# Optimization experiments

Hardware: AMD Instinct MI355X
Metric: run time of the kernel (lower is better)

Reference implementation:

```python
import jax, jax.numpy as jnp
import numpy as np

B, S, D_IN, D_H, D_OUT = 4, 2048, 512, 512, 512


def setup_inputs() -> dict:
    key = jax.random.key(0)
    ks = jax.random.split(key, 11)
    s_in = 1.0 / np.sqrt(D_IN)
    s_cat = 1.0 / np.sqrt(3 * D_H)
    return {
        "x1": jax.random.normal(ks[0], (B, S, D_IN), jnp.float32),
        "x2": jax.random.normal(ks[1], (B, S, D_IN), jnp.float32),
        "x3": jax.random.normal(ks[2], (B, S, D_IN), jnp.float32),
        "Wq": jax.random.normal(ks[3], (D_IN, D_H), jnp.float32) * s_in,
        "bq": jnp.zeros((D_H,), jnp.float32),
        "Wk": jax.random.normal(ks[4], (D_IN, D_H), jnp.float32) * s_in,
        "bk": jnp.zeros((D_H,), jnp.float32),
        "Wv": jax.random.normal(ks[5], (D_IN, D_H), jnp.float32) * s_in,
        "bv": jnp.zeros((D_H,), jnp.float32),
        "Wo": jax.random.normal(ks[6], (3 * D_H, D_OUT), jnp.float32) * s_cat,
        "bo": jnp.zeros((D_OUT,), jnp.float32),
    }


def _attn(Q, K, V):
    # Q: [B,S,H], K/V: [B,S,H] -> [B,S,H]
    scale = 1.0 / jnp.sqrt(jnp.asarray(K.shape[-1], Q.dtype))
    scores = jnp.einsum('bqh,bkh->bqk', Q, K) * scale
    w = jax.nn.softmax(scores, axis=-1)
    return jnp.einsum('bqk,bkh->bqh', w, V)


def reference(x1, x2, x3, Wq, bq, Wk, bk, Wv, bv, Wo, bo):
    Q1, Q2, Q3 = x1 @ Wq + bq, x2 @ Wq + bq, x3 @ Wq + bq
    K1, K2, K3 = x1 @ Wk + bk, x2 @ Wk + bk, x3 @ Wk + bk
    V1, V2, V3 = x1 @ Wv + bv, x2 @ Wv + bv, x3 @ Wv + bv
    fused_x1 = _attn(Q1, K2, V2) + _attn(Q1, K3, V3)
    fused_x2 = _attn(Q2, K1, V1) + _attn(Q2, K3, V3)
    fused_x3 = _attn(Q3, K1, V1) + _attn(Q3, K2, V2)
    fused = jnp.concatenate([fused_x1, fused_x2, fused_x3], axis=-1)
    return fused @ Wo + bo
```

## Files before the change

kernel.cpp:

```cpp
#include <hip/hip_runtime.h>
#include <hip/hip_bf16.h>

typedef __attribute__((ext_vector_type(4))) float  f32x4;
typedef __attribute__((ext_vector_type(8))) short  short8;

#define GAS(p) ((const __attribute__((address_space(1))) void*)(p))
#define LAS(p) ((__attribute__((address_space(3))) void*)(p))

__device__ inline short bf16_of(float f) {
    union { float f; unsigned u; } v; v.f = f;
    unsigned r = v.u + 0x7FFFu + ((v.u >> 16) & 1u);
    return (short)(r >> 16);
}

#define MFMA __builtin_amdgcn_mfma_f32_16x16x32_bf16

__device__ __forceinline__ void stage64(const short* A, long lda,
                                        const short* B, long ldb,
                                        short* As, short* Bs) {
    const int tid = threadIdx.x;
    const int w = tid >> 6, l = tid & 63;
    const int r = l >> 3;
    const int scol = ((l & 7) ^ r) * 8;
#pragma unroll
    for (int q = 0; q < 4; ++q) {
        const int rowb = q * 32 + w * 8;
        __builtin_amdgcn_global_load_lds(GAS(A + (long)(rowb + r) * lda + scol),
                                         LAS(As + rowb * 64), 16, 0, 0);
        __builtin_amdgcn_global_load_lds(GAS(B + (long)(rowb + r) * ldb + scol),
                                         LAS(Bs + rowb * 64), 16, 0, 0);
    }
}

__device__ __forceinline__ void gemm_core64(const short* A, long lda,
                                            const short* B, long ldb, int nk,
                                            short* sA, short* sB,
                                            f32x4 acc[4][4]) {
    const int tid = threadIdx.x;
    const int lane = tid & 63, wid = tid >> 6;
    const int wr = wid >> 1, wc = wid & 1;
    const int fr = lane & 15, fk = lane >> 4;
    const int swz = (fr & 7) << 4;
    const int abase = (wr * 64 + fr) * 128 + fk * 16;
    const int bbase = (wc * 64 + fr) * 128 + fk * 16;

    stage64(A, lda, B, ldb, sA, sB);
    __syncthreads();
    for (int ks = 0; ks < nk; ++ks) {
        const int cur = ks & 1;
        if (ks + 1 < nk)
            stage64(A + (ks + 1) * 64, lda, B + (ks + 1) * 64, ldb,
                    sA + (cur ^ 1) * 8192, sB + (cur ^ 1) * 8192);
        const char* pa = (const char*)(sA + cur * 8192);
        const char* pb = (const char*)(sB + cur * 8192);
        short8 af[2][4], bfr[2][4];
#pragma unroll
        for (int kk = 0; kk < 2; ++kk) {
#pragma unroll
            for (int mi = 0; mi < 4; ++mi)
                af[kk][mi] = *(const short8*)(pa + (((abase + kk * 64) ^ swz) + mi * 2048));
#pragma unroll
            for (int ni = 0; ni < 4; ++ni)
                bfr[kk][ni] = *(const short8*)(pb + (((bbase + kk * 64) ^ swz) + ni * 2048));
        }
#pragma unroll
        for (int kk = 0; kk < 2; ++kk)
#pragma unroll
            for (int mi = 0; mi < 4; ++mi)
#pragma unroll
                for (int ni = 0; ni < 4; ++ni)
                    acc[mi][ni] = MFMA(af[kk][mi], bfr[kk][ni], acc[mi][ni], 0, 0, 0);
        __syncthreads();
    }
}

__device__ __forceinline__ void bounce_store(short* Pb, const short vals[4][4][4],
                                             short* C, long ldc) {
    const int tid = threadIdx.x, lane = tid & 63, wid = tid >> 6;
    const int wr = wid >> 1, wc = wid & 1, fr = lane & 15, fk = lane >> 4;
#pragma unroll
    for (int mi = 0; mi < 4; ++mi)
#pragma unroll
        for (int ni = 0; ni < 4; ++ni)
#pragma unroll
            for (int r = 0; r < 4; ++r) {
                const int row = wr * 64 + mi * 16 + fk * 4 + r;
                const int col = wc * 64 + ni * 16 + fr;
                Pb[row * 128 + (col ^ ((row & 7) << 3))] = vals[mi][ni][r];
            }
    __syncthreads();
#pragma unroll
    for (int i = 0; i < 8; ++i) {
        const int row = i * 16 + (tid >> 4);
        const int ch = tid & 15;
        short8 v = *(const short8*)&Pb[row * 128 + ((ch * 8) ^ ((row & 7) << 3))];
        *(short8*)&C[(long)row * ldc + ch * 8] = v;
    }
}

__global__ __launch_bounds__(256, 2)
void proj_qk_k(const short* __restrict__ xb, const short* __restrict__ WqkT,
               short* __restrict__ Qb, short* __restrict__ Kb,
               const float* __restrict__ bq, const float* __restrict__ bk) {
    __shared__ short sA[2 * 8192], sB[2 * 8192];
    const short* Ab = xb + (long)blockIdx.x * 128 * 512;
    const short* Bb = WqkT + (long)blockIdx.y * 128 * 512;
    f32x4 acc[4][4] = {};
    gemm_core64(Ab, 512, Bb, 512, 8, sA, sB, acc);

    const int lane = threadIdx.x & 63, wid = threadIdx.x >> 6;
    const int wc = wid & 1, fr = lane & 15;
    const int qc0 = blockIdx.y * 128;
    const float* bias = qc0 < 512 ? bq + qc0 : bk + (qc0 - 512);
    short vals[4][4][4];
#pragma unroll
    for (int mi = 0; mi < 4; ++mi)
#pragma unroll
        for (int ni = 0; ni < 4; ++ni) {
            const float bv_ = bias[wc * 64 + ni * 16 + fr];
#pragma unroll
            for (int r = 0; r < 4; ++r)
                vals[mi][ni][r] = bf16_of(acc[mi][ni][r] + bv_);
        }
    short* dst = (qc0 < 512 ? Qb + qc0 : Kb + (qc0 - 512)) + (long)blockIdx.x * 128 * 512;
    bounce_store(sA, vals, dst, 512);
}

__global__ __launch_bounds__(256, 2)
void proj_vt_k(const short* __restrict__ WvT, const short* __restrict__ xb,
               short* __restrict__ VT, const float* __restrict__ bv) {
    __shared__ short sA[2 * 8192], sB[2 * 8192];
    const short* Ab = WvT + (long)blockIdx.x * 128 * 512;
    const short* Bb = xb + (long)blockIdx.y * 128 * 512;
    f32x4 acc[4][4] = {};
    gemm_core64(Ab, 512, Bb, 512, 8, sA, sB, acc);

    const int lane = threadIdx.x & 63, wid = threadIdx.x >> 6;
    const int wr = wid >> 1, fk = lane >> 4;
    short vals[4][4][4];
#pragma unroll
    for (int mi = 0; mi < 4; ++mi)
#pragma unroll
        for (int ni = 0; ni < 4; ++ni)
#pragma unroll
            for (int r = 0; r < 4; ++r) {
                const int rowg = blockIdx.x * 128 + wr * 64 + mi * 16 + fk * 4 + r;
                vals[mi][ni][r] = bf16_of(acc[mi][ni][r] + bv[rowg]);
            }
    bounce_store(sA, vals, VT + (long)blockIdx.x * 128 * 24576 + blockIdx.y * 128, 24576);
}

struct Off6 { long a[6], b[6]; };

__global__ __launch_bounds__(256, 4)
void qk_exp(const short* __restrict__ Qb, const short* __restrict__ Kb,
            short* __restrict__ Sc, float* __restrict__ lpart,
            Off6 o, int z0, int zmask, int zshift, float kscale) {
    __shared__ short lds[16384];
    short* As = lds;
    short* Bs = lds + 8192;
    const int bid = blockIdx.x;
    const int z = bid & zmask;
    const int t = bid >> zshift;
    const int bx = t & 15, by = t >> 4;
    const int slice = z0 + z;
    const int gp = slice >> 2, b = slice & 3;
    const short* A = Qb + o.a[gp] + ((long)b * 2048 + (long)bx * 128) * 512;
    const short* B = Kb + o.b[gp] + ((long)b * 2048 + (long)by * 128) * 512;

    const int tid = threadIdx.x, lane = tid & 63, wid = tid >> 6;
    const int wr = wid >> 1, wc = wid & 1, fr = lane & 15, fk = lane >> 4;
    const int sr = tid >> 2;
    const int scc = (((tid & 3) ^ (sr & 3)) * 8);
    const int arow = wr * 64 + fr, brow = wc * 64 + fr;

    auto stage = [&](const short* Ap, const short* Bp, int cur) {
        short* ad = As + cur * 4096;
        short* bd = Bs + cur * 4096;
        __builtin_amdgcn_global_load_lds(GAS(Ap + (long)sr * 512 + scc),
                                         LAS(ad + sr * 32 + (tid & 3) * 8), 16, 0, 0);
        __builtin_amdgcn_global_load_lds(GAS(Ap + (long)(sr + 64) * 512 + scc),
                                         LAS(ad + (sr + 64) * 32 + (tid & 3) * 8), 16, 0, 0);
        __builtin_amdgcn_global_load_lds(GAS(Bp + (long)sr * 512 + scc),
                                         LAS(bd + sr * 32 + (tid & 3) * 8), 16, 0, 0);
        __builtin_amdgcn_global_load_lds(GAS(Bp + (long)(sr + 64) * 512 + scc),
                                         LAS(bd + (sr + 64) * 32 + (tid & 3) * 8), 16, 0, 0);
    };

    f32x4 acc[4][4] = {};
    stage(A, B, 0);
    __syncthreads();
    for (int ks = 0; ks < 16; ++ks) {
        const int cur = ks & 1;
        if (ks + 1 < 16) stage(A + (ks + 1) * 32, B + (ks + 1) * 32, cur ^ 1);
        const short* pa = As + cur * 4096;
        const short* pb = Bs + cur * 4096;
        short8 af[4], bf[4];
#pragma unroll
        for (int mi = 0; mi < 4; ++mi) {
            const int row = arow + mi * 16;
            af[mi] = *(const short8*)&pa[row * 32 + ((fk ^ (row & 3)) * 8)];
        }
#pragma unroll
        for (int ni = 0; ni < 4; ++ni) {
            const int row = brow + ni * 16;
            bf[ni] = *(const short8*)&pb[row * 32 + ((fk ^ (row & 3)) * 8)];
        }
#pragma unroll
        for (int mi = 0; mi < 4; ++mi)
#pragma unroll
            for (int ni = 0; ni < 4; ++ni)
                acc[mi][ni] = MFMA(af[mi], bf[ni], acc[mi][ni], 0, 0, 0);
        __syncthreads();
    }

#pragma unroll
    for (int mi = 0; mi < 4; ++mi)
#pragma unroll
        for (int ni = 0; ni < 4; ++ni)
#pragma unroll
            for (int r = 0; r < 4; ++r)
                acc[mi][ni][r] = exp2f(acc[mi][ni][r] * kscale);

#pragma unroll
    for (int mi = 0; mi < 4; ++mi)
#pragma unroll
        for (int r = 0; r < 4; ++r) {
            float s = acc[mi][0][r] + acc[mi][1][r] + acc[mi][2][r] + acc[mi][3][r];
            s += __shfl_xor(s, 1); s += __shfl_xor(s, 2);
            s += __shfl_xor(s, 4); s += __shfl_xor(s, 8);
            if (fr == 0)
                lpart[((long)z * 32 + by * 2 + wc) * 2048 +
                      (long)bx * 128 + wr * 64 + mi * 16 + fk * 4 + r] = s;
        }

    short vals[4][4][4];
#pragma unroll
    for (int mi = 0; mi < 4; ++mi)
#pragma unroll
        for (int ni = 0; ni < 4; ++ni)
#pragma unroll
            for (int r = 0; r < 4; ++r)
                vals[mi][ni][r] = bf16_of(acc[mi][ni][r]);

    short* Cb = Sc + (long)z * 2048 * 2048 +
                (long)bx * 128 * 2048 + (long)by * 128;
    bounce_store(lds, vals, Cb, 2048);
}

struct POff { long v[6], c[6]; };

__global__ __launch_bounds__(256, 2)
void pv_div(const short* __restrict__ Sc, const short* __restrict__ VT,
            const float* __restrict__ lpart, short* __restrict__ F,
            POff o, int z0, int zmask, int zshift) {
    __shared__ short sA[2 * 8192], sB[2 * 8192];
    const int bid = blockIdx.x;
    const int z = bid & zmask;
    const int t = bid >> zshift;
    const int bx = t & 15, by = t >> 4;
    const int slice = z0 + z;
    const int gp = slice >> 2, b = slice & 3;
    const short* Ab = Sc + (long)z * 2048 * 2048 + (long)bx * 128 * 2048;
    const short* Bb = VT + o.v[gp] + (long)b * 2048 + (long)by * 128 * 24576;
    f32x4 acc[4][4] = {};
    gemm_core64(Ab, 2048, Bb, 24576, 32, sA, sB, acc);

    const int tid = threadIdx.x, lane = tid & 63, wid = tid >> 6;
    const int wr = wid >> 1, wc = wid & 1, fr = lane & 15, fk = lane >> 4;

    float* linv_s = (float*)sB;
    if (tid < 128) {
        const float* lp = lpart + ((long)z * 32) * 2048 + (long)bx * 128 + tid;
        float s = 0.f;
#pragma unroll
        for (int j = 0; j < 32; ++j) s += lp[(long)j * 2048];
        linv_s[tid] = 1.0f / s;
    }
    __syncthreads();

    short vals[4][4][4];
#pragma unroll
    for (int mi = 0; mi < 4; ++mi) {
        float linv[4];
#pragma unroll
        for (int r = 0; r < 4; ++r) linv[r] = linv_s[wr * 64 + mi * 16 + fk * 4 + r];
#pragma unroll
        for (int ni = 0; ni < 4; ++ni)
#pragma unroll
            for (int r = 0; r < 4; ++r)
                vals[mi][ni][r] = bf16_of(acc[mi][ni][r] * linv[r]);
    }
    __syncthreads();

    short* Cb = F + ((long)b * 2048 + (long)bx * 128) * 3072 +
                o.c[gp] + (long)by * 128;
    bounce_store(sA, vals, Cb, 3072);
}

__device__ __forceinline__ void stage_f(const short* A, const short* B,
                                        short* As, short* Bs) {
    const int tid = threadIdx.x, w = tid >> 6, l = tid & 63;
    const int r = l >> 3, scol = ((l & 7) ^ r) * 8;
#pragma unroll
    for (int q = 0; q < 4; ++q) {
        const int rowb = q * 32 + w * 8;
        __builtin_amdgcn_global_load_lds(GAS(A + (long)(rowb + r) * 3072 + scol),
                                         LAS(As + rowb * 64), 16, 0, 0);
    }
#pragma unroll
    for (int q = 0; q < 2; ++q) {
        const int rowb = q * 32 + w * 8;
        __builtin_amdgcn_global_load_lds(GAS(B + (long)(rowb + r) * 3072 + scol),
                                         LAS(Bs + rowb * 64), 16, 0, 0);
    }
}

__global__ __launch_bounds__(256, 3)
void final64(const short* __restrict__ A, const short* __restrict__ B,
             float* __restrict__ C, const float* __restrict__ bias) {
    __shared__ short sA[2 * 8192], sB[2 * 4096];
    const short* Ab = A + (long)blockIdx.x * 128 * 3072;
    const short* Bb = B + (long)blockIdx.y * 64 * 3072;
    const int tid = threadIdx.x, lane = tid & 63, w = tid >> 6;
    const int fr = lane & 15, fk = lane >> 4;
    const int swz = (fr & 7) << 4;
    const int abase = (w * 32 + fr) * 128 + fk * 16;
    const int bbase = fr * 128 + fk * 16;

    f32x4 acc[2][4] = {};
    stage_f(Ab, Bb, sA, sB);
    __syncthreads();
    for (int ks = 0; ks < 48; ++ks) {
        const int cur = ks & 1;
        if (ks + 1 < 48)
            stage_f(Ab + (ks + 1) * 64, Bb + (ks + 1) * 64,
                    sA + (cur ^ 1) * 8192, sB + (cur ^ 1) * 4096);
        const char* pa = (const char*)(sA + cur * 8192);
        const char* pb = (const char*)(sB + cur * 4096);
        short8 af[2][2], bf[2][4];
#pragma unroll
        for (int kk = 0; kk < 2; ++kk) {
#pragma unroll
            for (int mi = 0; mi < 2; ++mi)
                af[kk][mi] = *(const short8*)(pa + (((abase + kk * 64) ^ swz) + mi * 2048));
#pragma unroll
            for (int ni = 0; ni < 4; ++ni)
                bf[kk][ni] = *(const short8*)(pb + (((bbase + kk * 64) ^ swz) + ni * 2048));
        }
#pragma unroll
        for (int kk = 0; kk < 2; ++kk)
#pragma unroll
            for (int mi = 0; mi < 2; ++mi)
#pragma unroll
                for (int ni = 0; ni < 4; ++ni)
                    acc[mi][ni] = MFMA(af[kk][mi], bf[kk][ni], acc[mi][ni], 0, 0, 0);
        __syncthreads();
    }
    const long r0 = (long)blockIdx.x * 128 + w * 32 + fk * 4;
    const long c0 = (long)blockIdx.y * 64 + fr;
#pragma unroll
    for (int mi = 0; mi < 2; ++mi)
#pragma unroll
        for (int ni = 0; ni < 4; ++ni) {
            const long rr = r0 + mi * 16, cc = c0 + ni * 16;
#pragma unroll
            for (int r = 0; r < 4; ++r)
                C[(rr + r) * 512 + cc] = acc[mi][ni][r] + bias[cc];
        }
}

__global__ __launch_bounds__(256)
void xconv(const float* __restrict__ x0, const float* __restrict__ x1,
           const float* __restrict__ x2, short* __restrict__ xb) {
    const float* s = blockIdx.z == 0 ? x0 : (blockIdx.z == 1 ? x1 : x2);
    const long i = ((long)blockIdx.x * 256 + threadIdx.x) * 8;
    f32x4 a = *(const f32x4*)(s + i), c = *(const f32x4*)(s + i + 4);
    short8 v;
    v[0] = bf16_of(a.x); v[1] = bf16_of(a.y); v[2] = bf16_of(a.z); v[3] = bf16_of(a.w);
    v[4] = bf16_of(c.x); v[5] = bf16_of(c.y); v[6] = bf16_of(c.z); v[7] = bf16_of(c.w);
    *(short8*)(xb + (long)blockIdx.z * 8192 * 512 + i) = v;
}

__global__ __launch_bounds__(256)
void wprep(const float* __restrict__ Wq, const float* __restrict__ Wk,
           const float* __restrict__ Wv, const float* __restrict__ Wo,
           short* __restrict__ WqkT, short* __restrict__ WvT,
           short* __restrict__ WoT2) {
    __shared__ float t[32][33];
    const int z = blockIdx.z;
    const float* src; short* dst; int rows; long ldd; bool dup = false;
    if (z == 0)      { src = Wq; dst = WqkT;              rows = 512;  ldd = 512; }
    else if (z == 1) { src = Wk; dst = WqkT + 512L * 512; rows = 512;  ldd = 512; }
    else if (z == 2) { src = Wv; dst = WvT;               rows = 512;  ldd = 512; }
    else             { src = Wo; dst = WoT2;              rows = 1536; ldd = 3072; dup = true; }
    const int r0 = blockIdx.x * 32, c0 = blockIdx.y * 32;
    if (r0 >= rows) return;
    const int lx = threadIdx.x & 31, ly = threadIdx.x >> 5;
#pragma unroll
    for (int p = 0; p < 4; ++p)
        t[ly + 8 * p][lx] = src[(long)(r0 + ly + 8 * p) * 512 + (c0 + lx)];
    __syncthreads();
#pragma unroll
    for (int p = 0; p < 4; ++p) {
        const short v = bf16_of(t[lx][ly + 8 * p]);
        const long base = (long)(c0 + ly + 8 * p) * ldd + (r0 + lx);
        dst[base] = v;
        if (dup) dst[base + 1536] = v;
    }
}

extern "C" void kernel_launch(void* const* d_in, const int* in_sizes, int n_in,
                              void* d_out, int out_size, void* d_ws, size_t ws_size,
                              hipStream_t stream) {
    const float* x[3] = { (const float*)d_in[0], (const float*)d_in[1], (const float*)d_in[2] };
    const float* Wq = (const float*)d_in[3]; const float* bq = (const float*)d_in[4];
    const float* Wk = (const float*)d_in[5]; const float* bk = (const float*)d_in[6];
    const float* Wv = (const float*)d_in[7]; const float* bv = (const float*)d_in[8];
    const float* Wo = (const float*)d_in[9]; const float* bo = (const float*)d_in[10];

    const long TOK = 8192, T3 = 3 * TOK;

    char* ws = (char*)d_ws;
    size_t off = 0;
    auto alloc = [&](size_t bytes) -> void* {
        void* pp = ws + off;
        off += (bytes + 255) & ~(size_t)255;
        return pp;
    };

    short* WqkT  = (short*)alloc(1024L * 512 * 2);
    short* WvT   = (short*)alloc(512L * 512 * 2);
    short* WoT2  = (short*)alloc(512L * 3072 * 2);
    short* Qb    = (short*)alloc(T3 * 512 * 2);
    short* Kb    = (short*)alloc(T3 * 512 * 2);
    short* VT    = (short*)alloc(512L * T3 * 2);
    short* fused = (short*)alloc(TOK * 3072 * 2);
    float* lpart = (float*)alloc(8L * 32 * 2048 * 4);
    short* xb    = (short*)alloc(T3 * 512 * 2);

    const size_t SLICE = 2048L * 2048 * 2;
    const size_t rem = ws_size > off ? ws_size - off : 0;
    const int nsl = (rem >= 8 * SLICE) ? 8 : 4;
    const int zshift = (nsl == 8) ? 3 : 2;
    short* scores = (short*)alloc((size_t)nsl * SLICE);

    const dim3 tb(256);
    wprep<<<dim3(48, 16, 4), tb, 0, stream>>>(Wq, Wk, Wv, Wo, WqkT, WvT, WoT2);
    xconv<<<dim3(2048, 1, 3), tb, 0, stream>>>(x[0], x[1], x[2], xb);

    proj_qk_k<<<dim3(192, 8), tb, 0, stream>>>(xb, WqkT, Qb, Kb, bq, bk);
    proj_vt_k<<<dim3(4, 192), tb, 0, stream>>>(WvT, xb, VT, bv);

    const int imap[6] = {0, 1, 2, 0, 1, 2};
    const int jmap[6] = {1, 0, 0, 2, 2, 1};
    Off6 qo{}; POff po{};
    for (int gp = 0; gp < 6; ++gp) {
        qo.a[gp] = (long)imap[gp] * TOK * 512;
        qo.b[gp] = (long)jmap[gp] * TOK * 512;
        po.v[gp] = (long)jmap[gp] * TOK;
        po.c[gp] = (long)imap[gp] * 512 + (gp >= 3 ? 1536 : 0);
    }
    const float kscale = 0.04419417382415922f * 1.4426950408889634f;

    for (int z0 = 0; z0 < 24; z0 += nsl) {
        qk_exp<<<dim3(256 * nsl), tb, 0, stream>>>(Qb, Kb, scores, lpart, qo,
                                                   z0, nsl - 1, zshift, kscale);
        pv_div<<<dim3(64 * nsl), tb, 0, stream>>>(scores, VT, lpart, fused, po,
                                                  z0, nsl - 1, zshift);
    }

    final64<<<dim3(64, 8), tb, 0, stream>>>(fused, WoT2, (float*)d_out, bo);
}
```

Before: 401.0 us.

## Enlarge QK^T exp tile to 256x128 per block with custom LDS epilogue

The qk_exp kernel now computes a 256x128 score tile per block instead of 128x128, with each wave holding 8x4 MFMA accumulators, so the K tile is loaded once for twice as many query rows. The grid is halved, LDS grows to 48KB and occupancy hint drops from 4 to 2 blocks per CU. The epilogue writes bf16 scores through a swizzled LDS bounce in two halves, replacing the previous bounce_store helper. The intent is to cut global/LDS traffic per MFMA, at the cost of higher register pressure and lower occupancy.

```diff
diff --git a/kernel.cpp b/kernel.cpp
--- a/kernel.cpp
+++ b/kernel.cpp
@@ -152,62 +152,65 @@
 
 struct Off6 { long a[6], b[6]; };
 
-__global__ __launch_bounds__(256, 4)
+__global__ __launch_bounds__(256, 2)
 void qk_exp(const short* __restrict__ Qb, const short* __restrict__ Kb,
             short* __restrict__ Sc, float* __restrict__ lpart,
             Off6 o, int z0, int zmask, int zshift, float kscale) {
-    __shared__ short lds[16384];
+    __shared__ short lds[24576];
     short* As = lds;
-    short* Bs = lds + 8192;
+    short* Bs = lds + 16384;
     const int bid = blockIdx.x;
     const int z = bid & zmask;
     const int t = bid >> zshift;
-    const int bx = t & 15, by = t >> 4;
+    const int bx = t & 7, by = t >> 3;
     const int slice = z0 + z;
     const int gp = slice >> 2, b = slice & 3;
-    const short* A = Qb + o.a[gp] + ((long)b * 2048 + (long)bx * 128) * 512;
+    const short* A = Qb + o.a[gp] + ((long)b * 2048 + (long)bx * 256) * 512;
     const short* B = Kb + o.b[gp] + ((long)b * 2048 + (long)by * 128) * 512;
 
     const int tid = threadIdx.x, lane = tid & 63, wid = tid >> 6;
     const int wr = wid >> 1, wc = wid & 1, fr = lane & 15, fk = lane >> 4;
-    const int sr = tid >> 2;
-    const int scc = (((tid & 3) ^ (sr & 3)) * 8);
-    const int arow = wr * 64 + fr, brow = wc * 64 + fr;
+    const int sr = tid >> 2, c4 = tid & 3;
+    const int scc = ((c4 ^ (sr & 3)) * 8);
 
     auto stage = [&](const short* Ap, const short* Bp, int cur) {
-        short* ad = As + cur * 4096;
+        short* ad = As + cur * 8192;
         short* bd = Bs + cur * 4096;
-        __builtin_amdgcn_global_load_lds(GAS(Ap + (long)sr * 512 + scc),
-                                         LAS(ad + sr * 32 + (tid & 3) * 8), 16, 0, 0);
-        __builtin_amdgcn_global_load_lds(GAS(Ap + (long)(sr + 64) * 512 + scc),
-                                         LAS(ad + (sr + 64) * 32 + (tid & 3) * 8), 16, 0, 0);
-        __builtin_amdgcn_global_load_lds(GAS(Bp + (long)sr * 512 + scc),
-                                         LAS(bd + sr * 32 + (tid & 3) * 8), 16, 0, 0);
-        __builtin_amdgcn_global_load_lds(GAS(Bp + (long)(sr + 64) * 512 + scc),
-                                         LAS(bd + (sr + 64) * 32 + (tid & 3) * 8), 16, 0, 0);
+#pragma unroll
+        for (int q = 0; q < 4; ++q) {
+            const int row = sr + q * 64;
+            __builtin_amdgcn_global_load_lds(GAS(Ap + (long)row * 512 + scc),
+                                             LAS(ad + row * 32 + c4 * 8), 16, 0, 0);
+        }
+#pragma unroll
+        for (int q = 0; q < 2; ++q) {
+            const int row = sr + q * 64;
+            __builtin_amdgcn_global_load_lds(GAS(Bp + (long)row * 512 + scc),
+                                             LAS(bd + row * 32 + c4 * 8), 16, 0, 0);
+        }
     };
 
-    f32x4 acc[4][4] = {};
+    f32x4 acc[8][4] = {};
     stage(A, B, 0);
     __syncthreads();
     for (int ks = 0; ks < 16; ++ks) {
         const int cur = ks & 1;
         if (ks + 1 < 16) stage(A + (ks + 1) * 32, B + (ks + 1) * 32, cur ^ 1);
-        const short* pa = As + cur * 4096;
+        const short* pa = As + cur * 8192;
         const short* pb = Bs + cur * 4096;
-        short8 af[4], bf[4];
-#pragma unroll
-        for (int mi = 0; mi < 4; ++mi) {
-            const int row = arow + mi * 16;
+        short8 af[8], bf[4];
+#pragma unroll
+        for (int mi = 0; mi < 8; ++mi) {
+            const int row = wr * 128 + mi * 16 + fr;
             af[mi] = *(const short8*)&pa[row * 32 + ((fk ^ (row & 3)) * 8)];
         }
 #pragma unroll
         for (int ni = 0; ni < 4; ++ni) {
-            const int row = brow + ni * 16;
+            const int row = wc * 64 + ni * 16 + fr;
             bf[ni] = *(const short8*)&pb[row * 32 + ((fk ^ (row & 3)) * 8)];
         }
 #pragma unroll
-        for (int mi = 0; mi < 4; ++mi)
+        for (int mi = 0; mi < 8; ++mi)
 #pragma unroll
             for (int ni = 0; ni < 4; ++ni)
                 acc[mi][ni] = MFMA(af[mi], bf[ni], acc[mi][ni], 0, 0, 0);
@@ -215,7 +218,7 @@
     }
 
 #pragma unroll
-    for (int mi = 0; mi < 4; ++mi)
+    for (int mi = 0; mi < 8; ++mi)
 #pragma unroll
         for (int ni = 0; ni < 4; ++ni)
 #pragma unroll
@@ -223,7 +226,7 @@
                 acc[mi][ni][r] = exp2f(acc[mi][ni][r] * kscale);
 
 #pragma unroll
-    for (int mi = 0; mi < 4; ++mi)
+    for (int mi = 0; mi < 8; ++mi)
 #pragma unroll
         for (int r = 0; r < 4; ++r) {
             float s = acc[mi][0][r] + acc[mi][1][r] + acc[mi][2][r] + acc[mi][3][r];
@@ -231,21 +234,34 @@
             s += __shfl_xor(s, 4); s += __shfl_xor(s, 8);
             if (fr == 0)
                 lpart[((long)z * 32 + by * 2 + wc) * 2048 +
-                      (long)bx * 128 + wr * 64 + mi * 16 + fk * 4 + r] = s;
-        }
-
-    short vals[4][4][4];
-#pragma unroll
-    for (int mi = 0; mi < 4; ++mi)
-#pragma unroll
-        for (int ni = 0; ni < 4; ++ni)
-#pragma unroll
-            for (int r = 0; r < 4; ++r)
-                vals[mi][ni][r] = bf16_of(acc[mi][ni][r]);
-
-    short* Cb = Sc + (long)z * 2048 * 2048 +
-                (long)bx * 128 * 2048 + (long)by * 128;
-    bounce_store(lds, vals, Cb, 2048);
+                      (long)bx * 256 + wr * 128 + mi * 16 + fk * 4 + r] = s;
+        }
+
+    short* Cb = Sc + (long)z * 2048 * 2048 + (long)bx * 256 * 2048 + (long)by * 128;
+#pragma unroll
+    for (int h = 0; h < 2; ++h) {
+        __syncthreads();
+        if (wr == h) {
+#pragma unroll
+            for (int mi = 0; mi < 8; ++mi)
+#pragma unroll
+                for (int ni = 0; ni < 4; ++ni)
+#pragma unroll
+                    for (int r = 0; r < 4; ++r) {
+                        const int row = mi * 16 + fk * 4 + r;
+                        const int col = wc * 64 + ni * 16 + fr;
+                        lds[row * 128 + (col ^ ((row & 7) << 3))] = bf16_of(acc[mi][ni][r]);
+                    }
+        }
+        __syncthreads();
+#pragma unroll
+        for (int i = 0; i < 8; ++i) {
+            const int row = i * 16 + (tid >> 4);
+            const int ch = tid & 15;
+            short8 v = *(const short8*)&lds[row * 128 + ((ch * 8) ^ ((row & 7) << 3))];
+            *(short8*)&Cb[(long)(h * 128 + row) * 2048 + ch * 8] = v;
+        }
+    }
 }
 
 struct POff { long v[6], c[6]; };
@@ -464,7 +480,7 @@
     const float kscale = 0.04419417382415922f * 1.4426950408889634f;
 
     for (int z0 = 0; z0 < 24; z0 += nsl) {
-        qk_exp<<<dim3(256 * nsl), tb, 0, stream>>>(Qb, Kb, scores, lpart, qo,
+        qk_exp<<<dim3(128 * nsl), tb, 0, stream>>>(Qb, Kb, scores, lpart, qo,
                                                    z0, nsl - 1, zshift, kscale);
         pv_div<<<dim3(64 * nsl), tb, 0, stream>>>(scores, VT, lpart, fused, po,
                                                   z0, nsl - 1, zshift);
```

New measurement: 419.0 us. 1.04x slower.

## Triple-buffer LDS staging in qk_exp with vmcnt-based waits and one barrier

Applied to the files above, without the earlier changes.

Moves the QK^T score kernel's LDS staging from two buffers to three. Loads run two k-steps ahead, and each iteration waits with s_waitcnt vmcnt(4) plus a single barrier instead of two __syncthreads. The goal is to hide more global-load latency behind the MFMAs and remove one barrier per step. The extra LDS (48KB per block) lowers the launch-bounds occupancy hint from 4 to 3 blocks.

```diff
diff --git a/kernel.cpp b/kernel.cpp
--- a/kernel.cpp
+++ b/kernel.cpp
@@ -152,13 +152,11 @@
 
 struct Off6 { long a[6], b[6]; };
 
-__global__ __launch_bounds__(256, 4)
+__global__ __launch_bounds__(256, 3)
 void qk_exp(const short* __restrict__ Qb, const short* __restrict__ Kb,
             short* __restrict__ Sc, float* __restrict__ lpart,
             Off6 o, int z0, int zmask, int zshift, float kscale) {
-    __shared__ short lds[16384];
-    short* As = lds;
-    short* Bs = lds + 8192;
+    __shared__ short lds[24576];
     const int bid = blockIdx.x;
     const int z = bid & zmask;
     const int t = bid >> zshift;
@@ -170,31 +168,35 @@
 
     const int tid = threadIdx.x, lane = tid & 63, wid = tid >> 6;
     const int wr = wid >> 1, wc = wid & 1, fr = lane & 15, fk = lane >> 4;
-    const int sr = tid >> 2;
-    const int scc = (((tid & 3) ^ (sr & 3)) * 8);
+    const int sr = tid >> 2, c4 = tid & 3;
+    const int scc = ((c4 ^ (sr & 3)) * 8);
     const int arow = wr * 64 + fr, brow = wc * 64 + fr;
 
-    auto stage = [&](const short* Ap, const short* Bp, int cur) {
-        short* ad = As + cur * 4096;
-        short* bd = Bs + cur * 4096;
+    auto stage = [&](const short* Ap, const short* Bp, int slot) {
+        short* ad = lds + slot * 8192;
+        short* bd = ad + 4096;
         __builtin_amdgcn_global_load_lds(GAS(Ap + (long)sr * 512 + scc),
-                                         LAS(ad + sr * 32 + (tid & 3) * 8), 16, 0, 0);
+                                         LAS(ad + sr * 32 + c4 * 8), 16, 0, 0);
         __builtin_amdgcn_global_load_lds(GAS(Ap + (long)(sr + 64) * 512 + scc),
-                                         LAS(ad + (sr + 64) * 32 + (tid & 3) * 8), 16, 0, 0);
+                                         LAS(ad + (sr + 64) * 32 + c4 * 8), 16, 0, 0);
         __builtin_amdgcn_global_load_lds(GAS(Bp + (long)sr * 512 + scc),
-                                         LAS(bd + sr * 32 + (tid & 3) * 8), 16, 0, 0);
+                                         LAS(bd + sr * 32 + c4 * 8), 16, 0, 0);
         __builtin_amdgcn_global_load_lds(GAS(Bp + (long)(sr + 64) * 512 + scc),
-                                         LAS(bd + (sr + 64) * 32 + (tid & 3) * 8), 16, 0, 0);
+                                         LAS(bd + (sr + 64) * 32 + c4 * 8), 16, 0, 0);
     };
 
     f32x4 acc[4][4] = {};
     stage(A, B, 0);
-    __syncthreads();
+    stage(A + 32, B + 32, 1);
+
     for (int ks = 0; ks < 16; ++ks) {
-        const int cur = ks & 1;
-        if (ks + 1 < 16) stage(A + (ks + 1) * 32, B + (ks + 1) * 32, cur ^ 1);
-        const short* pa = As + cur * 4096;
-        const short* pb = Bs + cur * 4096;
+        if (ks < 15) asm volatile("s_waitcnt vmcnt(4)" ::: "memory");
+        else         asm volatile("s_waitcnt vmcnt(0)" ::: "memory");
+        __builtin_amdgcn_sched_barrier(0);
+        __builtin_amdgcn_s_barrier();
+        const short* pa = lds + (ks % 3) * 8192;
+        const short* pb = pa + 4096;
+        if (ks + 2 < 16) stage(A + (ks + 2) * 32, B + (ks + 2) * 32, (ks + 2) % 3);
         short8 af[4], bf[4];
 #pragma unroll
         for (int mi = 0; mi < 4; ++mi) {
@@ -211,8 +213,8 @@
 #pragma unroll
             for (int ni = 0; ni < 4; ++ni)
                 acc[mi][ni] = MFMA(af[mi], bf[ni], acc[mi][ni], 0, 0, 0);
-        __syncthreads();
-    }
+    }
+    __syncthreads();
 
 #pragma unroll
     for (int mi = 0; mi < 4; ++mi)
```

Result: no change. 403.8 us (+0.7%).
